# Optimization experiments

Measured on AMD Instinct MI355X. Metric: run time of the kernel, lower is better.

## Reference

```python
import jax, jax.numpy as jnp
import numpy as np

PAD = 0
SOS = 1
NEG = -1e9


def _lstm_scan(x, Wih, Whh, b, h0, c0, reverse=False):
    # x: [T, B, in]; torch gate order i, f, g, o
    def step(carry, xt):
        h, c = carry
        g = xt @ Wih.T + h @ Whh.T + b
        i, f, gg, o = jnp.split(g, 4, axis=-1)
        c = jax.nn.sigmoid(f) * c + jax.nn.sigmoid(i) * jnp.tanh(gg)
        h = jax.nn.sigmoid(o) * jnp.tanh(c)
        return (h, c), h
    (hT, cT), hs = jax.lax.scan(step, (h0, c0), x, reverse=reverse)
    return hs, hT, cT


def setup_inputs() -> dict:
    B, Ts, Tt = 32, 64, 66
    E, H, V = 512, 512, 16000
    key = jax.random.key(0)
    ks = jax.random.split(key, 16)
    s = 0.05
    n = lambda k, shape: (jax.random.normal(k, shape, dtype=jnp.float32) * s)
    return {
        'src_sentences': jax.random.randint(ks[0], (B, Ts), 4, V),
        'trg_sentences': jax.random.randint(ks[1], (B, Tt), 4, V),
        'src_emb': n(ks[2], (V, E)),
        'trg_emb': n(ks[3], (V, E)),
        'enc0_Wih': n(ks[4], (2, 4 * H, E)),
        'enc0_Whh': n(ks[5], (2, 4 * H, H)),
        'enc0_b': n(ks[6], (2, 4 * H)),
        'enc1_Wih': n(ks[7], (2, 4 * H, 2 * H)),
        'enc1_Whh': n(ks[8], (2, 4 * H, H)),
        'enc1_b': n(ks[9], (2, 4 * H)),
        'dec_Wih': n(ks[10], (8 * H, E)),      # LSTMCell: hidden = 2H -> 4*(2H) gates
        'dec_Whh': n(ks[11], (8 * H, 2 * H)),
        'dec_b': n(ks[12], (8 * H)),
        'out_W1': n(ks[13], (H, 4 * H)),
        'out_W2': n(ks[14], (V - 4, H)),
    }


def reference(src_sentences, trg_sentences, src_emb, trg_emb,
              enc0_Wih, enc0_Whh, enc0_b, enc1_Wih, enc1_Whh, enc1_b,
              dec_Wih, dec_Whh, dec_b, out_W1, out_W2):
    B, Ts = src_sentences.shape
    Tt = trg_sentences.shape[1]
    H = out_W1.shape[0]
    dt = src_emb.dtype
    enc_mask = src_sentences == PAD            # [B, Ts] (all False here)

    # ---- encoder: 2-layer bidirectional LSTM (dropout inactive / eval) ----
    x = jnp.swapaxes(src_emb[src_sentences], 0, 1)   # [Ts, B, E]
    z = jnp.zeros((B, H), dt)
    hf0, hfT, cfT = _lstm_scan(x, enc0_Wih[0], enc0_Whh[0], enc0_b[0], z, z)
    hb0, hbT, cbT = _lstm_scan(x, enc0_Wih[1], enc0_Whh[1], enc0_b[1], z, z, reverse=True)
    x1 = jnp.concatenate([hf0, hb0], axis=-1)        # [Ts, B, 2H]
    hf1, _, _ = _lstm_scan(x1, enc1_Wih[0], enc1_Whh[0], enc1_b[0], z, z)
    hb1, _, _ = _lstm_scan(x1, enc1_Wih[1], enc1_Whh[1], enc1_b[1], z, z, reverse=True)
    enc_out = jnp.swapaxes(jnp.concatenate([hf1, hb1], axis=-1), 0, 1)  # [B, Ts, 2H]
    # module uses encoder_hidden_t[0], [1] -> layer-0 fwd/bwd final states
    hidden = jnp.concatenate([hfT, hbT], axis=-1)    # [B, 2H]
    cell = jnp.concatenate([cfT, cbT], axis=-1)

    # ---- decoder: teacher_force = 1.0 (deterministic) ----
    steps = Tt - 2
    emb_in = jnp.swapaxes(trg_emb[trg_sentences[:, :steps]], 0, 1)  # [steps, B, E]
    tgts = jnp.swapaxes(trg_sentences[:, 1:steps + 1], 0, 1)        # [steps, B]

    def step(carry, inp):
        h, c, loss = carry
        xt, tgt = inp
        g = xt @ dec_Wih.T + h @ dec_Whh.T + dec_b
        i, f, gg, o = jnp.split(g, 4, axis=-1)
        c = jax.nn.sigmoid(f) * c + jax.nn.sigmoid(i) * jnp.tanh(gg)
        h = jax.nn.sigmoid(o) * jnp.tanh(c)
        dmask = tgt == PAD
        h = jnp.where(dmask[:, None], jnp.zeros((), dt), h)  # decoder_hidden_t[mask] = 0
        # dot attention over encoder states
        scores = jnp.einsum('btd,bd->bt', enc_out, h)
        scores = jnp.where(enc_mask, NEG, scores)
        attn = jax.nn.softmax(scores, axis=1)
        ctx = jnp.einsum('bt,btd->bd', attn, enc_out)
        zt = jnp.tanh(jnp.concatenate([h, ctx], axis=-1) @ out_W1.T)
        logits = zt @ out_W2.T                                # [B, V-4]
        logp = jax.nn.log_softmax(logits, axis=1)
        tgt_idx = tgt - 4
        valid = tgt_idx != -4                                 # ignore_index=-4 (PAD)
        safe = jnp.where(valid, tgt_idx, 0)
        nll = -jnp.take_along_axis(logp, safe[:, None], axis=1)[:, 0]
        loss = loss + jnp.sum(jnp.where(valid, nll, jnp.zeros((), dt)))
        pred = jnp.argmax(logits, axis=1) + 4
        return (h, c, loss), pred

    (_, _, loss), preds = jax.lax.scan(step, (hidden, cell, jnp.zeros((), dt)), (emb_in, tgts))
    denom = jnp.sum(trg_sentences[:, 1:-1] != PAD).astype(dt)
    return loss / denom, preds.T  # preds: [B, steps]
```

## Files before the change

### kernel.cpp

```cpp
#include <hip/hip_runtime.h>
#include <hip/hip_bf16.h>
#include <math.h>

#define TSRC 64
#define TTRG 66
#define NVOC 15996
#define NTILE 125

__device__ __forceinline__ float sigm(float x){ return 1.f/(1.f+expf(-x)); }

__global__ __launch_bounds__(256)
void k_gemm128(const float* __restrict__ A, int lda,
               const float* __restrict__ Bw, int ldb,
               const float* __restrict__ bias,
               float* __restrict__ C, int ldc, int K, int nNb)
{
  const int tid = threadIdx.x;
  const int mb = blockIdx.x / nNb;
  const int nb = blockIdx.x % nNb;
  const int m0 = mb*128, n0 = nb*128;

  __shared__ alignas(16) float As[16][132];
  __shared__ alignas(16) float Bs[16][132];
  const int tx = tid & 15;
  const int ty = tid >> 4;
  float acc[8][8];
  #pragma unroll
  for (int i=0;i<8;i++)
    #pragma unroll
    for (int j=0;j<8;j++) acc[i][j]=0.f;

  for (int kt=0; kt<K; kt+=16) {
    #pragma unroll
    for (int i=tid; i<128*16; i+=256) {
      int m = i>>4, k = i&15;
      As[k][m] = A[(size_t)(m0+m)*lda + kt + k];
    }
    #pragma unroll
    for (int i=tid; i<128*16; i+=256) {
      int n = i>>4, k = i&15;
      Bs[k][n] = Bw[(size_t)(n0+n)*ldb + kt + k];
    }
    __syncthreads();
    #pragma unroll
    for (int k=0;k<16;k++) {
      float4 a0 = *reinterpret_cast<const float4*>(&As[k][ty*4]);
      float4 a1 = *reinterpret_cast<const float4*>(&As[k][64+ty*4]);
      float4 b0 = *reinterpret_cast<const float4*>(&Bs[k][tx*4]);
      float4 b1 = *reinterpret_cast<const float4*>(&Bs[k][64+tx*4]);
      float av[8] = {a0.x,a0.y,a0.z,a0.w,a1.x,a1.y,a1.z,a1.w};
      float bv[8] = {b0.x,b0.y,b0.z,b0.w,b1.x,b1.y,b1.z,b1.w};
      #pragma unroll
      for (int i=0;i<8;i++)
        #pragma unroll
        for (int j=0;j<8;j++)
          acc[i][j] = fmaf(av[i], bv[j], acc[i][j]);
    }
    __syncthreads();
  }
  #pragma unroll
  for (int i=0;i<8;i++) {
    int m = m0 + ((i<4) ? ty*4+i : 64+ty*4+(i-4));
    int nA = n0 + tx*4, nB = n0 + 64 + tx*4;
    float4 v0, v1;
    v0.x = acc[i][0] + (bias?bias[nA+0]:0.f);
    v0.y = acc[i][1] + (bias?bias[nA+1]:0.f);
    v0.z = acc[i][2] + (bias?bias[nA+2]:0.f);
    v0.w = acc[i][3] + (bias?bias[nA+3]:0.f);
    v1.x = acc[i][4] + (bias?bias[nB+0]:0.f);
    v1.y = acc[i][5] + (bias?bias[nB+1]:0.f);
    v1.z = acc[i][6] + (bias?bias[nB+2]:0.f);
    v1.w = acc[i][7] + (bias?bias[nB+3]:0.f);
    *reinterpret_cast<float4*>(&C[(size_t)m*ldc + nA]) = v0;
    *reinterpret_cast<float4*>(&C[(size_t)m*ldc + nB]) = v1;
  }
}

__global__ __launch_bounds__(256)
void k_logits(const float* __restrict__ A, const float* __restrict__ Bw,
              const int* __restrict__ trg,
              float* __restrict__ Pmax, int* __restrict__ Parg,
              float* __restrict__ Psum, float* __restrict__ Ltgt)
{
  const int tid = threadIdx.x;
  const int j8   = blockIdx.x & 7;
  const int mb   = (blockIdx.x >> 3) & 15;
  const int nb   = ((blockIdx.x >> 7) << 3) + j8;
  if (nb >= NTILE) return;
  const int m0 = mb*128, n0 = nb*128;

  __shared__ alignas(16) float As[16][132];
  __shared__ alignas(16) float Bs[16][132];
  const int tx = tid & 15;
  const int ty = tid >> 4;
  float acc[8][8];
  #pragma unroll
  for (int i=0;i<8;i++)
    #pragma unroll
    for (int j=0;j<8;j++) acc[i][j]=0.f;

  for (int kt=0; kt<512; kt+=16) {
    #pragma unroll
    for (int i=tid; i<128*16; i+=256) {
      int m = i>>4, k = i&15;
      As[k][m] = A[(size_t)(m0+m)*512 + kt + k];
    }
    #pragma unroll
    for (int i=tid; i<128*16; i+=256) {
      int n = i>>4, k = i&15;
      int gn = n0+n;
      Bs[k][n] = (gn < NVOC) ? Bw[(size_t)gn*512 + kt + k] : 0.f;
    }
    __syncthreads();
    #pragma unroll
    for (int k=0;k<16;k++) {
      float4 a0 = *reinterpret_cast<const float4*>(&As[k][ty*4]);
      float4 a1 = *reinterpret_cast<const float4*>(&As[k][64+ty*4]);
      float4 b0 = *reinterpret_cast<const float4*>(&Bs[k][tx*4]);
      float4 b1 = *reinterpret_cast<const float4*>(&Bs[k][64+tx*4]);
      float av[8] = {a0.x,a0.y,a0.z,a0.w,a1.x,a1.y,a1.z,a1.w};
      float bv[8] = {b0.x,b0.y,b0.z,b0.w,b1.x,b1.y,b1.z,b1.w};
      #pragma unroll
      for (int i=0;i<8;i++)
        #pragma unroll
        for (int j=0;j<8;j++)
          acc[i][j] = fmaf(av[i], bv[j], acc[i][j]);
    }
    __syncthreads();
  }

  #pragma unroll
  for (int i=0;i<8;i++) {
    int r = m0 + ((i<4) ? ty*4+i : 64+ty*4+(i-4));
    int step = r >> 5, b = r & 31;
    int tgt = trg[b*TTRG + step + 1];
    int ti = tgt - 4;
    float m = -3.4e38f; int am = 0x7fffffff;
    #pragma unroll
    for (int j=0;j<8;j++) {
      int gn = n0 + ((j<4) ? tx*4+j : 64+tx*4+(j-4));
      if (gn < NVOC) {
        float x = acc[i][j];
        if (x > m || (x == m && gn < am)) { m = x; am = gn; }
      }
    }
    float s = 0.f;
    float lt = 0.f;
    #pragma unroll
    for (int j=0;j<8;j++) {
      int gn = n0 + ((j<4) ? tx*4+j : 64+tx*4+(j-4));
      if (gn < NVOC) {
        s += expf(acc[i][j] - m);
        if (gn == ti) lt = acc[i][j];
      }
    }
    #pragma unroll
    for (int d=1; d<16; d<<=1) {
      float m2 = __shfl_xor(m, d);
      int   a2 = __shfl_xor(am, d);
      float s2 = __shfl_xor(s, d);
      float l2 = __shfl_xor(lt, d);
      float M = fmaxf(m, m2);
      s = s*expf(m - M) + s2*expf(m2 - M);
      if (m2 > m || (m2 == m && a2 < am)) am = a2;
      m = M;
      lt += l2;
    }
    if (tx == 0) {
      size_t pi = (size_t)r*NTILE + nb;
      Pmax[pi] = m; Parg[pi] = am; Psum[pi] = s;
      if (ti >= n0 && ti < n0 + 128) Ltgt[r] = lt;
    }
  }
}

struct GArgs {
  const float* A;  int lda;
  const float* Bw; int ldb;
  const float* bias;
  float* C; int ldc;
  int N; int K; int nNb; int act;
};

template<int BM,int BN,int BK,int TM,int TN>
__global__ __launch_bounds__(256)
void k_gemm(GArgs a)
{
  const int tid = threadIdx.x;
  const int mb = blockIdx.x / a.nNb;
  const int nb = blockIdx.x % a.nNb;
  const int m0 = mb*BM, n0 = nb*BN;
  const float* A  = a.A + (size_t)m0*a.lda;
  const float* Bw = a.Bw;

  __shared__ float As[BK][BM+1];
  __shared__ float Bs[BK][BN+4];
  const int tx = tid % (BN/TN);
  const int ty = tid / (BN/TN);
  float acc[TM][TN];
  #pragma unroll
  for (int i=0;i<TM;i++)
    #pragma unroll
    for (int j=0;j<TN;j++) acc[i][j]=0.f;

  for (int kt=0; kt<a.K; kt+=BK) {
    #pragma unroll
    for (int i=tid; i<BM*BK; i+=256) {
      int m = i/BK, k = i%BK;
      As[k][m] = A[(size_t)m*a.lda + kt + k];
    }
    #pragma unroll
    for (int i=tid; i<BN*BK; i+=256) {
      int n = i/BK, k = i%BK;
      int gn = n0+n;
      Bs[k][n] = (gn < a.N) ? Bw[(size_t)gn*a.ldb + kt + k] : 0.f;
    }
    __syncthreads();
    #pragma unroll
    for (int k=0;k<BK;k++) {
      float av[TM], bv[TN];
      #pragma unroll
      for (int i=0;i<TM;i++) av[i]=As[k][ty*TM+i];
      #pragma unroll
      for (int j=0;j<TN;j++) bv[j]=Bs[k][tx*TN+j];
      #pragma unroll
      for (int i=0;i<TM;i++)
        #pragma unroll
        for (int j=0;j<TN;j++)
          acc[i][j] = fmaf(av[i], bv[j], acc[i][j]);
    }
    __syncthreads();
  }
  #pragma unroll
  for (int i=0;i<TM;i++) {
    int m = m0 + ty*TM + i;
    #pragma unroll
    for (int j=0;j<TN;j++) {
      int n = n0 + tx*TN + j;
      if (n < a.N) {
        float v = acc[i][j];
        if (a.bias) v += a.bias[n];
        if (a.act)  v = tanhf(v);
        a.C[(size_t)m*a.ldc + n] = v;
      }
    }
  }
}

__global__ __launch_bounds__(128)
void k_combine(const float* __restrict__ Pmax, const int* __restrict__ Parg,
               const float* __restrict__ Psum, const float* __restrict__ Ltgt,
               const int* __restrict__ trg,
               float* __restrict__ nll, float* __restrict__ outp)
{
  int r = blockIdx.x;
  int step = r >> 5, b = r & 31;
  int tid = threadIdx.x;
  __shared__ float sm[128]; __shared__ int sa[128]; __shared__ float ssum[128];
  float m = -3.4e38f; int am = 0x7fffffff; float s = 0.f;
  if (tid < NTILE) {
    size_t pi = (size_t)r*NTILE + tid;
    m = Pmax[pi]; am = Parg[pi]; s = Psum[pi];
  }
  sm[tid]=m; sa[tid]=am; ssum[tid]=s; __syncthreads();
  for (int off=64; off; off>>=1) {
    if (tid < off) {
      float m2 = sm[tid+off]; int a2 = sa[tid+off]; float s2 = ssum[tid+off];
      float m1 = sm[tid];     int a1 = sa[tid];     float s1 = ssum[tid];
      float M = fmaxf(m1, m2);
      ssum[tid] = s1*expf(m1 - M) + s2*expf(m2 - M);
      if (m2 > m1 || (m2 == m1 && a2 < a1)) sa[tid] = a2;
      sm[tid] = M;
    }
    __syncthreads();
  }
  if (tid == 0) {
    int tgt = trg[b*TTRG + step + 1];
    float nl = 0.f;
    if (tgt != 0) nl = -(Ltgt[r] - sm[0] - logf(ssum[0]));
    nll[step*32 + b] = nl;
    outp[1 + b*64 + step] = (float)(sa[0] + 4);
  }
}

__global__ void k_gather(const float* __restrict__ emb, const int* __restrict__ tok,
                         float* __restrict__ outp, int Tfull)
{
  int r = blockIdx.x;
  int t = r >> 5, b = r & 31;
  int token = tok[b*Tfull + t];
  const float4* s = (const float4*)(emb + (size_t)token*512);
  float4* d = (float4*)(outp + (size_t)r*512);
  d[threadIdx.x] = s[threadIdx.x];
}

__global__ __launch_bounds__(256)
void k_estep(const float* __restrict__ Whh,
             const float* __restrict__ xg,
             const float* __restrict__ hin,
             float* __restrict__ hout,
             float* __restrict__ cst,
             float* __restrict__ xout, int s, int mode)
{
  const int bid = blockIdx.x;
  const int dir = bid >> 7;
  const int j0  = (bid & 127) * 4;
  const int tid = threadIdx.x;
  const int kg  = tid >> 5;
  const int b   = tid & 31;
  __shared__ float4 wl4[16*128];
  __shared__ float red[4*16*33];

  {
    const float* W = Whh + (size_t)dir*2048*512;
    for (int idx = tid; idx < 16*128; idx += 256) {
      int r = idx >> 7, c = idx & 127;
      int g = r >> 2, jj = r & 3;
      wl4[idx] = ((const float4*)(W + (size_t)(g*512 + j0 + jj)*512))[c];
    }
  }
  float4 hreg[16];
  {
    const float4* H4 = (const float4*)(hin + (size_t)dir*32*512);
    #pragma unroll
    for (int j=0;j<16;j++) hreg[j] = H4[(size_t)b*128 + kg*16 + j];
  }
  __syncthreads();

  float acc[16];
  #pragma unroll
  for (int r=0;r<16;r++) {
    const float4* wr = wl4 + r*128 + kg*16;
    float a0=0.f,a1=0.f,a2=0.f,a3=0.f;
    #pragma unroll
    for (int j=0;j<16;j++) {
      float4 w = wr[j];
      a0 = fmaf(w.x, hreg[j].x, a0);
      a1 = fmaf(w.y, hreg[j].y, a1);
      a2 = fmaf(w.z, hreg[j].z, a2);
      a3 = fmaf(w.w, hreg[j].w, a3);
    }
    acc[r] = (a0+a1)+(a2+a3);
  }
  #pragma unroll
  for (int r=0;r<16;r++) acc[r] += __shfl_xor(acc[r], 32);
  const int wv = tid >> 6;
  if ((tid & 32) == 0) {
    #pragma unroll
    for (int r=0;r<16;r++) red[wv*528 + r*33 + b] = acc[r];
  }
  __syncthreads();

  if (tid < 128) {
    int jj = tid >> 5, bb = tid & 31;
    int jh = j0 + jj;
    int t  = dir ? (63 - s) : s;
    const float* x = xg + ((size_t)t*32 + bb)*4096 + dir*2048;
    float g4[4];
    #pragma unroll
    for (int g=0; g<4; g++) {
      int r = g*4 + jj;
      g4[g] = ((red[0*528 + r*33 + bb] + red[1*528 + r*33 + bb])
             + (red[2*528 + r*33 + bb] + red[3*528 + r*33 + bb]))
             + x[g*512 + jh];
    }
    size_t ci = ((size_t)dir*32 + bb)*512 + jh;
    float cn = sigm(g4[1])*cst[ci] + sigm(g4[0])*tanhf(g4[2]);
    float hn = sigm(g4[3])*tanhf(cn);
    cst[ci] = cn;
    hout[ci] = hn;
    if (mode == 0) xout[((size_t)t*32 + bb)*1024 + dir*512 + jh] = hn;
    else           xout[((size_t)bb*64 + t)*1024 + dir*512 + jh] = hn;
  }
}

__global__ __launch_bounds__(256)
void k_dstep(const float* __restrict__ Whh,
             const float* __restrict__ xg_t,
             const float* __restrict__ hin,
             float* __restrict__ cst,
             float* __restrict__ hall_t,
             const int* __restrict__ trg, int st)
{
  const int bid = blockIdx.x;
  const int j0  = bid*4;
  const int tid = threadIdx.x;
  const int kg  = tid >> 5;
  const int b   = tid & 31;
  __shared__ float4 wl4[8*256];
  __shared__ float red[4*16*33];

  float4 hreg[32];
  {
    const float4* H4 = (const float4*)hin;
    #pragma unroll
    for (int j=0;j<32;j++) hreg[j] = H4[(size_t)b*256 + kg*32 + j];
  }

  float acc[16];
  #pragma unroll
  for (int hh=0; hh<2; hh++) {
    for (int idx = tid; idx < 8*256; idx += 256) {
      int rl = idx >> 8, c = idx & 255;
      int r = hh*8 + rl;
      int g = r >> 2, jj = r & 3;
      wl4[idx] = ((const float4*)(Whh + (size_t)(g*1024 + j0 + jj)*1024))[c];
    }
    __syncthreads();
    #pragma unroll
    for (int rl=0; rl<8; rl++) {
      const float4* wr = wl4 + rl*256 + kg*32;
      float a0=0.f,a1=0.f,a2=0.f,a3=0.f;
      #pragma unroll
      for (int j=0;j<32;j++) {
        float4 w = wr[j];
        a0 = fmaf(w.x, hreg[j].x, a0);
        a1 = fmaf(w.y, hreg[j].y, a1);
        a2 = fmaf(w.z, hreg[j].z, a2);
        a3 = fmaf(w.w, hreg[j].w, a3);
      }
      acc[hh*8 + rl] = (a0+a1)+(a2+a3);
    }
    __syncthreads();
  }
  #pragma unroll
  for (int r=0;r<16;r++) acc[r] += __shfl_xor(acc[r], 32);
  const int wv = tid >> 6;
  if ((tid & 32) == 0) {
    #pragma unroll
    for (int r=0;r<16;r++) red[wv*528 + r*33 + b] = acc[r];
  }
  __syncthreads();

  if (tid < 128) {
    int jj = tid >> 5, bb = tid & 31;
    int jh = j0 + jj;
    int tgt = trg[bb*TTRG + st + 1];
    bool dm = (tgt == 0);
    const float* x = xg_t + (size_t)bb*4096;
    float g4[4];
    #pragma unroll
    for (int g=0; g<4; g++) {
      int r = g*4 + jj;
      g4[g] = ((red[0*528 + r*33 + bb] + red[1*528 + r*33 + bb])
             + (red[2*528 + r*33 + bb] + red[3*528 + r*33 + bb]))
             + x[g*1024 + jh];
    }
    size_t ci = (size_t)bb*1024 + jh;
    float cn = sigm(g4[1])*cst[ci] + sigm(g4[0])*tanhf(g4[2]);
    float hn = sigm(g4[3])*tanhf(cn);
    cst[ci] = cn;
    hall_t[ci] = dm ? 0.f : hn;
  }
}

__global__ void k_pack(const float* __restrict__ hfin, const float* __restrict__ cfin,
                       float* __restrict__ dh, float* __restrict__ dcc)
{
  int tid = blockIdx.x*256 + threadIdx.x;
  int j = tid & 1023, b = tid >> 10;
  int dir = j >> 9, jj = j & 511;
  size_t si = ((size_t)dir*32 + b)*512 + jj;
  dh[(size_t)b*1024 + j]  = hfin[si];
  dcc[(size_t)b*1024 + j] = cfin[si];
}

__global__ __launch_bounds__(256)
void k_attn(const float* __restrict__ Hall,
            const float* __restrict__ encout,
            const int* __restrict__ src,
            float* __restrict__ hctx)
{
  int bid = blockIdx.x;
  int t = bid >> 5, b = bid & 31;
  int tid = threadIdx.x;
  __shared__ float sh[1024];
  __shared__ float ssc[64];
  const float* h = Hall + ((size_t)t*32 + b)*1024;
  size_t row = (size_t)t*32 + b;
  #pragma unroll
  for (int r=0;r<4;r++) {
    int jh = tid + 256*r;
    float v = h[jh];
    sh[jh] = v;
    hctx[row*2048 + jh] = v;
  }
  __syncthreads();
  {
    int tq = tid >> 2, part = tid & 3;
    const float* eo = encout + ((size_t)b*64 + tq)*1024 + part*256;
    const float* hh = sh + part*256;
    float s = 0.f;
    for (int k=0;k<256;k++) s = fmaf(hh[k], eo[k], s);
    s += __shfl_xor(s, 1);
    s += __shfl_xor(s, 2);
    if (part == 0) ssc[tq] = (src[b*TSRC + tq] == 0) ? -1e9f : s;
  }
  __syncthreads();
  if (tid < 64) {
    float v = ssc[tid];
    float m = v;
    for (int d=1; d<64; d<<=1) m = fmaxf(m, __shfl_xor(m, d));
    float e = expf(v - m);
    float su = e;
    for (int d=1; d<64; d<<=1) su += __shfl_xor(su, d);
    ssc[tid] = e / su;
  }
  __syncthreads();
  #pragma unroll
  for (int r=0;r<4;r++) {
    int k = tid + 256*r;
    float a = 0.f;
    const float* eb = encout + (size_t)b*65536 + k;
    for (int tt=0;tt<64;tt++) a = fmaf(ssc[tt], eb[tt*1024], a);
    hctx[row*2048 + 1024 + k] = a;
  }
}

__global__ __launch_bounds__(256)
void k_final(const float* __restrict__ nll, const int* __restrict__ trg,
             float* __restrict__ outp)
{
  int tid = threadIdx.x;
  __shared__ float ss[256]; __shared__ int sc[256];
  float s = 0.f; int cnt = 0;
  for (int i=tid; i<2048; i+=256) {
    s += nll[i];
    int b = i >> 6, t = (i & 63) + 1;
    cnt += (trg[b*TTRG + t] != 0);
  }
  ss[tid]=s; sc[tid]=cnt; __syncthreads();
  for (int off=128; off; off>>=1) {
    if (tid<off) { ss[tid]+=ss[tid+off]; sc[tid]+=sc[tid+off]; }
    __syncthreads();
  }
  if (tid==0) outp[0] = ss[0] / (float)sc[0];
}

static void launch_big(hipStream_t st, const float* A, int lda,
                       const float* Bw, int ldb, const float* bias,
                       float* C, int ldc, int M, int N, int K)
{
  int nNb = N/128;
  dim3 g((M/128)*nNb, 1, 1);
  k_gemm128<<<g, dim3(256), 0, st>>>(A, lda, Bw, ldb, bias, C, ldc, K, nNb);
}

static void launch_med(hipStream_t st, const float* A, int lda,
                       const float* Bw, int ldb, const float* bias,
                       float* C, int ldc, int M, int N, int K, int act)
{
  GArgs a;
  a.A=A; a.lda=lda;
  a.Bw=Bw; a.ldb=ldb;
  a.bias=bias;
  a.C=C; a.ldc=ldc;
  a.N=N; a.K=K; a.nNb=(N+63)/64; a.act=act;
  dim3 g((M/64)*a.nNb, 1, 1);
  k_gemm<64,64,16,4,4><<<g, dim3(256), 0, st>>>(a);
}

extern "C" void kernel_launch(void* const* d_in, const int* in_sizes, int n_in,
                              void* d_out, int out_size, void* d_ws, size_t ws_size,
                              hipStream_t stream)
{
  (void)in_sizes; (void)n_in; (void)out_size; (void)ws_size;
  const int*   src   = (const int*)  d_in[0];
  const int*   trg   = (const int*)  d_in[1];
  const float* semb  = (const float*)d_in[2];
  const float* temb  = (const float*)d_in[3];
  const float* e0Wih = (const float*)d_in[4];
  const float* e0Whh = (const float*)d_in[5];
  const float* e0b   = (const float*)d_in[6];
  const float* e1Wih = (const float*)d_in[7];
  const float* e1Whh = (const float*)d_in[8];
  const float* e1b   = (const float*)d_in[9];
  const float* dWih  = (const float*)d_in[10];
  const float* dWhh  = (const float*)d_in[11];
  const float* db    = (const float*)d_in[12];
  const float* W1    = (const float*)d_in[13];
  const float* W2    = (const float*)d_in[14];
  float* out = (float*)d_out;

  float* ws = (float*)d_ws;
  size_t o = 0;
  float* x_in   = ws + o; o += (size_t)2048*512;
  float* xg     = ws + o; o += (size_t)2048*4096;
  float* x1     = ws + o; o += (size_t)2048*1024;
  float* encout = ws + o; o += (size_t)2048*1024;
  float* hA     = ws + o; o += 2*32*512;
  float* hB     = ws + o; o += 2*32*512;
  float* cbuf   = ws + o; o += 2*32*512;
  float* dh0    = ws + o; o += 32*1024;
  float* dc     = ws + o; o += 32*1024;
  float* nll    = ws + o; o += 2048;
  float* Hall   = x1;
  float* hctx   = xg;
  float* zt     = x_in;
  float* Pmax   = xg + (size_t)4*1024*1024;
  int*   Parg   = (int*)(Pmax + (size_t)2048*NTILE);
  float* Psum   = Pmax + (size_t)2*2048*NTILE;
  float* Ltgt   = Pmax + (size_t)3*2048*NTILE;

  hipMemsetAsync(hA,   0, 2*32*512*sizeof(float), stream);
  hipMemsetAsync(cbuf, 0, 2*32*512*sizeof(float), stream);
  k_gather<<<dim3(2048), dim3(128), 0, stream>>>(semb, src, x_in, TSRC);
  launch_big(stream, x_in, 512, e0Wih, 512, e0b, xg, 4096, 2048, 4096, 512);
  for (int s=0; s<64; s++) {
    float* hin  = (s&1) ? hB : hA;
    float* hout = (s&1) ? hA : hB;
    k_estep<<<dim3(256), dim3(256), 0, stream>>>(e0Whh, xg, hin, hout, cbuf, x1, s, 0);
  }
  k_pack<<<dim3(128), dim3(256), 0, stream>>>(hA, cbuf, dh0, dc);

  hipMemsetAsync(hA,   0, 2*32*512*sizeof(float), stream);
  hipMemsetAsync(cbuf, 0, 2*32*512*sizeof(float), stream);
  launch_big(stream, x1, 1024, e1Wih, 1024, e1b, xg, 4096, 2048, 4096, 1024);
  for (int s=0; s<64; s++) {
    float* hin  = (s&1) ? hB : hA;
    float* hout = (s&1) ? hA : hB;
    k_estep<<<dim3(256), dim3(256), 0, stream>>>(e1Whh, xg, hin, hout, cbuf, encout, s, 1);
  }

  k_gather<<<dim3(2048), dim3(128), 0, stream>>>(temb, trg, x_in, TTRG);
  launch_big(stream, x_in, 512, dWih, 512, db, xg, 4096, 2048, 4096, 512);
  for (int st=0; st<64; st++) {
    const float* hin = (st == 0) ? dh0 : (Hall + (size_t)(st-1)*32*1024);
    k_dstep<<<dim3(256), dim3(256), 0, stream>>>(dWhh, xg + (size_t)st*32*4096,
                 hin, dc, Hall + (size_t)st*32*1024, trg, st);
  }

  k_attn<<<dim3(2048), dim3(256), 0, stream>>>(Hall, encout, src, hctx);
  launch_med(stream, hctx, 2048, W1, 2048, nullptr, zt, 512, 2048, 512, 2048, 1);
  k_logits<<<dim3(2048), dim3(256), 0, stream>>>(zt, W2, trg, Pmax, Parg, Psum, Ltgt);
  k_combine<<<dim3(2048), dim3(128), 0, stream>>>(Pmax, Parg, Psum, Ltgt, trg, nll, out);
  k_final<<<dim3(1), dim3(256), 0, stream>>>(nll, trg, out);
}
```

Measured before the change: 4.118 ms.

## Fuse encoder layer-1 and decoder recurrent steps into one concurrent kernel

The decoder recurrence depends only on layer-0 final states and target embeddings, so it is now run alongside the encoder layer-1 recurrence in a single 512-block launch per step. Encoder blocks take the first 256 block ids and decoder blocks the rest. This halves the number of serial step launches and lets the two recurrences share the GPU. The decoder input projection (x·Wih) is computed inside each step instead of by a separate large GEMM, which adds per-step weight loads and FMAs to every decoder step.

```diff
diff --git a/kernel.cpp b/kernel.cpp
--- a/kernel.cpp
+++ b/kernel.cpp
@@ -300,7 +300,7 @@
              const float* __restrict__ hin,
              float* __restrict__ hout,
              float* __restrict__ cst,
-             float* __restrict__ xout, int s, int mode)
+             float* __restrict__ xout, int s)
 {
   const int bid = blockIdx.x;
   const int dir = bid >> 7;
@@ -369,88 +369,184 @@
     float hn = sigm(g4[3])*tanhf(cn);
     cst[ci] = cn;
     hout[ci] = hn;
-    if (mode == 0) xout[((size_t)t*32 + bb)*1024 + dir*512 + jh] = hn;
-    else           xout[((size_t)bb*64 + t)*1024 + dir*512 + jh] = hn;
+    xout[((size_t)t*32 + bb)*1024 + dir*512 + jh] = hn;
   }
 }
 
 __global__ __launch_bounds__(256)
-void k_dstep(const float* __restrict__ Whh,
-             const float* __restrict__ xg_t,
-             const float* __restrict__ hin,
-             float* __restrict__ cst,
-             float* __restrict__ hall_t,
-             const int* __restrict__ trg, int st)
-{
-  const int bid = blockIdx.x;
-  const int j0  = bid*4;
+void k_mstep(const float* __restrict__ eWhh,
+             const float* __restrict__ xg,
+             const float* __restrict__ ehin, float* __restrict__ ehout,
+             float* __restrict__ ecst,
+             float* __restrict__ encout,
+             const float* __restrict__ dWhh,
+             const float* __restrict__ dWih,
+             const float* __restrict__ db,
+             const float* __restrict__ xemb,
+             const float* __restrict__ dhin,
+             float* __restrict__ dcst,
+             float* __restrict__ dhall_t,
+             const int* __restrict__ trg, int s)
+{
   const int tid = threadIdx.x;
   const int kg  = tid >> 5;
   const int b   = tid & 31;
-  __shared__ float4 wl4[8*256];
+  __shared__ float4 wl4[2048];
   __shared__ float red[4*16*33];
 
-  float4 hreg[32];
-  {
-    const float4* H4 = (const float4*)hin;
-    #pragma unroll
-    for (int j=0;j<32;j++) hreg[j] = H4[(size_t)b*256 + kg*32 + j];
-  }
-
-  float acc[16];
-  #pragma unroll
-  for (int hh=0; hh<2; hh++) {
-    for (int idx = tid; idx < 8*256; idx += 256) {
-      int rl = idx >> 8, c = idx & 255;
-      int r = hh*8 + rl;
-      int g = r >> 2, jj = r & 3;
-      wl4[idx] = ((const float4*)(Whh + (size_t)(g*1024 + j0 + jj)*1024))[c];
-    }
-    __syncthreads();
-    #pragma unroll
-    for (int rl=0; rl<8; rl++) {
-      const float4* wr = wl4 + rl*256 + kg*32;
+  if (blockIdx.x < 256) {
+    const int dir = blockIdx.x >> 7;
+    const int j0  = (blockIdx.x & 127) * 4;
+    {
+      const float* W = eWhh + (size_t)dir*2048*512;
+      for (int idx = tid; idx < 16*128; idx += 256) {
+        int r = idx >> 7, c = idx & 127;
+        int g = r >> 2, jj = r & 3;
+        wl4[idx] = ((const float4*)(W + (size_t)(g*512 + j0 + jj)*512))[c];
+      }
+    }
+    float4 hreg[16];
+    {
+      const float4* H4 = (const float4*)(ehin + (size_t)dir*32*512);
+      #pragma unroll
+      for (int j=0;j<16;j++) hreg[j] = H4[(size_t)b*128 + kg*16 + j];
+    }
+    __syncthreads();
+
+    float acc[16];
+    #pragma unroll
+    for (int r=0;r<16;r++) {
+      const float4* wr = wl4 + r*128 + kg*16;
       float a0=0.f,a1=0.f,a2=0.f,a3=0.f;
       #pragma unroll
-      for (int j=0;j<32;j++) {
+      for (int j=0;j<16;j++) {
         float4 w = wr[j];
         a0 = fmaf(w.x, hreg[j].x, a0);
         a1 = fmaf(w.y, hreg[j].y, a1);
         a2 = fmaf(w.z, hreg[j].z, a2);
         a3 = fmaf(w.w, hreg[j].w, a3);
       }
-      acc[hh*8 + rl] = (a0+a1)+(a2+a3);
-    }
-    __syncthreads();
-  }
-  #pragma unroll
-  for (int r=0;r<16;r++) acc[r] += __shfl_xor(acc[r], 32);
-  const int wv = tid >> 6;
-  if ((tid & 32) == 0) {
-    #pragma unroll
-    for (int r=0;r<16;r++) red[wv*528 + r*33 + b] = acc[r];
-  }
-  __syncthreads();
-
-  if (tid < 128) {
-    int jj = tid >> 5, bb = tid & 31;
-    int jh = j0 + jj;
-    int tgt = trg[bb*TTRG + st + 1];
-    bool dm = (tgt == 0);
-    const float* x = xg_t + (size_t)bb*4096;
-    float g4[4];
-    #pragma unroll
-    for (int g=0; g<4; g++) {
-      int r = g*4 + jj;
-      g4[g] = ((red[0*528 + r*33 + bb] + red[1*528 + r*33 + bb])
-             + (red[2*528 + r*33 + bb] + red[3*528 + r*33 + bb]))
-             + x[g*1024 + jh];
-    }
-    size_t ci = (size_t)bb*1024 + jh;
-    float cn = sigm(g4[1])*cst[ci] + sigm(g4[0])*tanhf(g4[2]);
-    float hn = sigm(g4[3])*tanhf(cn);
-    cst[ci] = cn;
-    hall_t[ci] = dm ? 0.f : hn;
+      acc[r] = (a0+a1)+(a2+a3);
+    }
+    #pragma unroll
+    for (int r=0;r<16;r++) acc[r] += __shfl_xor(acc[r], 32);
+    const int wv = tid >> 6;
+    if ((tid & 32) == 0) {
+      #pragma unroll
+      for (int r=0;r<16;r++) red[wv*528 + r*33 + b] = acc[r];
+    }
+    __syncthreads();
+
+    if (tid < 128) {
+      int jj = tid >> 5, bb = tid & 31;
+      int jh = j0 + jj;
+      int t  = dir ? (63 - s) : s;
+      const float* x = xg + ((size_t)t*32 + bb)*4096 + dir*2048;
+      float g4[4];
+      #pragma unroll
+      for (int g=0; g<4; g++) {
+        int r = g*4 + jj;
+        g4[g] = ((red[0*528 + r*33 + bb] + red[1*528 + r*33 + bb])
+               + (red[2*528 + r*33 + bb] + red[3*528 + r*33 + bb]))
+               + x[g*512 + jh];
+      }
+      size_t ci = ((size_t)dir*32 + bb)*512 + jh;
+      float cn = sigm(g4[1])*ecst[ci] + sigm(g4[0])*tanhf(g4[2]);
+      float hn = sigm(g4[3])*tanhf(cn);
+      ecst[ci] = cn;
+      ehout[ci] = hn;
+      encout[((size_t)bb*64 + t)*1024 + dir*512 + jh] = hn;
+    }
+  } else {
+    const int j0 = (blockIdx.x - 256) * 4;
+    for (int idx = tid; idx < 16*128; idx += 256) {
+      int r = idx >> 7, c = idx & 127;
+      int g = r >> 2, jj = r & 3;
+      wl4[idx] = ((const float4*)(dWih + (size_t)(g*1024 + j0 + jj)*512))[c];
+    }
+    float4 xreg[16];
+    {
+      const float4* X4 = (const float4*)(xemb + (size_t)s*32*512);
+      #pragma unroll
+      for (int j=0;j<16;j++) xreg[j] = X4[(size_t)b*128 + kg*16 + j];
+    }
+    float4 hreg[32];
+    {
+      const float4* H4 = (const float4*)dhin;
+      #pragma unroll
+      for (int j=0;j<32;j++) hreg[j] = H4[(size_t)b*256 + kg*32 + j];
+    }
+    __syncthreads();
+
+    float acc[16];
+    #pragma unroll
+    for (int r=0;r<16;r++) {
+      const float4* wr = wl4 + r*128 + kg*16;
+      float a0=0.f,a1=0.f,a2=0.f,a3=0.f;
+      #pragma unroll
+      for (int j=0;j<16;j++) {
+        float4 w = wr[j];
+        a0 = fmaf(w.x, xreg[j].x, a0);
+        a1 = fmaf(w.y, xreg[j].y, a1);
+        a2 = fmaf(w.z, xreg[j].z, a2);
+        a3 = fmaf(w.w, xreg[j].w, a3);
+      }
+      acc[r] = (a0+a1)+(a2+a3);
+    }
+    __syncthreads();
+    #pragma unroll
+    for (int hh=0; hh<2; hh++) {
+      for (int idx = tid; idx < 8*256; idx += 256) {
+        int rl = idx >> 8, c = idx & 255;
+        int r = hh*8 + rl;
+        int g = r >> 2, jj = r & 3;
+        wl4[idx] = ((const float4*)(dWhh + (size_t)(g*1024 + j0 + jj)*1024))[c];
+      }
+      __syncthreads();
+      #pragma unroll
+      for (int rl=0; rl<8; rl++) {
+        const float4* wr = wl4 + rl*256 + kg*32;
+        float a0=0.f,a1=0.f,a2=0.f,a3=0.f;
+        #pragma unroll
+        for (int j=0;j<32;j++) {
+          float4 w = wr[j];
+          a0 = fmaf(w.x, hreg[j].x, a0);
+          a1 = fmaf(w.y, hreg[j].y, a1);
+          a2 = fmaf(w.z, hreg[j].z, a2);
+          a3 = fmaf(w.w, hreg[j].w, a3);
+        }
+        acc[hh*8 + rl] += (a0+a1)+(a2+a3);
+      }
+      __syncthreads();
+    }
+    #pragma unroll
+    for (int r=0;r<16;r++) acc[r] += __shfl_xor(acc[r], 32);
+    const int wv = tid >> 6;
+    if ((tid & 32) == 0) {
+      #pragma unroll
+      for (int r=0;r<16;r++) red[wv*528 + r*33 + b] = acc[r];
+    }
+    __syncthreads();
+
+    if (tid < 128) {
+      int jj = tid >> 5, bb = tid & 31;
+      int jh = j0 + jj;
+      int tgt = trg[bb*TTRG + s + 1];
+      bool dm = (tgt == 0);
+      float g4[4];
+      #pragma unroll
+      for (int g=0; g<4; g++) {
+        int r = g*4 + jj;
+        g4[g] = ((red[0*528 + r*33 + bb] + red[1*528 + r*33 + bb])
+               + (red[2*528 + r*33 + bb] + red[3*528 + r*33 + bb]))
+               + db[g*1024 + jh];
+      }
+      size_t ci = (size_t)bb*1024 + jh;
+      float cn = sigm(g4[1])*dcst[ci] + sigm(g4[0])*tanhf(g4[2]);
+      float hn = sigm(g4[3])*tanhf(cn);
+      dcst[ci] = cn;
+      dhall_t[ci] = dm ? 0.f : hn;
+    }
   }
 }
 
@@ -609,25 +705,22 @@
   for (int s=0; s<64; s++) {
     float* hin  = (s&1) ? hB : hA;
     float* hout = (s&1) ? hA : hB;
-    k_estep<<<dim3(256), dim3(256), 0, stream>>>(e0Whh, xg, hin, hout, cbuf, x1, s, 0);
+    k_estep<<<dim3(256), dim3(256), 0, stream>>>(e0Whh, xg, hin, hout, cbuf, x1, s);
   }
   k_pack<<<dim3(128), dim3(256), 0, stream>>>(hA, cbuf, dh0, dc);
 
   hipMemsetAsync(hA,   0, 2*32*512*sizeof(float), stream);
   hipMemsetAsync(cbuf, 0, 2*32*512*sizeof(float), stream);
   launch_big(stream, x1, 1024, e1Wih, 1024, e1b, xg, 4096, 2048, 4096, 1024);
+  k_gather<<<dim3(2048), dim3(128), 0, stream>>>(temb, trg, x_in, TTRG);
+
   for (int s=0; s<64; s++) {
-    float* hin  = (s&1) ? hB : hA;
-    float* hout = (s&1) ? hA : hB;
-    k_estep<<<dim3(256), dim3(256), 0, stream>>>(e1Whh, xg, hin, hout, cbuf, encout, s, 1);
-  }
-
-  k_gather<<<dim3(2048), dim3(128), 0, stream>>>(temb, trg, x_in, TTRG);
-  launch_big(stream, x_in, 512, dWih, 512, db, xg, 4096, 2048, 4096, 512);
-  for (int st=0; st<64; st++) {
-    const float* hin = (st == 0) ? dh0 : (Hall + (size_t)(st-1)*32*1024);
-    k_dstep<<<dim3(256), dim3(256), 0, stream>>>(dWhh, xg + (size_t)st*32*4096,
-                 hin, dc, Hall + (size_t)st*32*1024, trg, st);
+    float* ehin  = (s&1) ? hB : hA;
+    float* ehout = (s&1) ? hA : hB;
+    const float* dhin = (s == 0) ? dh0 : (Hall + (size_t)(s-1)*32*1024);
+    k_mstep<<<dim3(512), dim3(256), 0, stream>>>(
+        e1Whh, xg, ehin, ehout, cbuf, encout,
+        dWhh, dWih, db, x_in, dhin, dc, Hall + (size_t)s*32*1024, trg, s);
   }
 
   k_attn<<<dim3(2048), dim3(256), 0, stream>>>(Hall, encout, src, hctx);
```

After: 4.742 ms. +15.1%, slower.

## Double-buffer shared-memory tiles in fp32 GEMM and logits kernels

Applied to the files above, without the earlier changes.

Both tiled fp32 GEMM kernels (the generic one and the fused vocabulary-logits one) now keep two shared-memory stages. The next K-slice is prefetched into registers while the current slice is multiplied, then written to the other buffer. This halves the barriers per K step and hides global-load latency behind the FMA loop. The cost is doubled LDS use and 16 extra registers per thread, which may lower occupancy.

```diff
diff --git a/kernel.cpp b/kernel.cpp
--- a/kernel.cpp
+++ b/kernel.cpp
@@ -20,34 +20,45 @@
   const int nb = blockIdx.x % nNb;
   const int m0 = mb*128, n0 = nb*128;
 
-  __shared__ alignas(16) float As[16][132];
-  __shared__ alignas(16) float Bs[16][132];
+  __shared__ alignas(16) float As[2][16][132];
+  __shared__ alignas(16) float Bs[2][16][132];
   const int tx = tid & 15;
   const int ty = tid >> 4;
+  const int sm_ = tid >> 4;
+  const int sk_ = tid & 15;
   float acc[8][8];
   #pragma unroll
   for (int i=0;i<8;i++)
     #pragma unroll
     for (int j=0;j<8;j++) acc[i][j]=0.f;
 
-  for (int kt=0; kt<K; kt+=16) {
-    #pragma unroll
-    for (int i=tid; i<128*16; i+=256) {
-      int m = i>>4, k = i&15;
-      As[k][m] = A[(size_t)(m0+m)*lda + kt + k];
-    }
-    #pragma unroll
-    for (int i=tid; i<128*16; i+=256) {
-      int n = i>>4, k = i&15;
-      Bs[k][n] = Bw[(size_t)(n0+n)*ldb + kt + k];
-    }
-    __syncthreads();
+  #pragma unroll
+  for (int q=0;q<8;q++) {
+    int m = sm_ + 16*q;
+    As[0][sk_][m] = A[(size_t)(m0+m)*lda + sk_];
+    Bs[0][sk_][m] = Bw[(size_t)(n0+m)*ldb + sk_];
+  }
+  __syncthreads();
+
+  const int NT = K >> 4;
+  for (int t=0; t<NT; ++t) {
+    int cur = t & 1, nxt = cur^1;
+    float aR[8], bR[8];
+    if (t+1 < NT) {
+      int kt = (t+1)<<4;
+      #pragma unroll
+      for (int q=0;q<8;q++) {
+        int m = sm_ + 16*q;
+        aR[q] = A[(size_t)(m0+m)*lda + kt + sk_];
+        bR[q] = Bw[(size_t)(n0+m)*ldb + kt + sk_];
+      }
+    }
     #pragma unroll
     for (int k=0;k<16;k++) {
-      float4 a0 = *reinterpret_cast<const float4*>(&As[k][ty*4]);
-      float4 a1 = *reinterpret_cast<const float4*>(&As[k][64+ty*4]);
-      float4 b0 = *reinterpret_cast<const float4*>(&Bs[k][tx*4]);
-      float4 b1 = *reinterpret_cast<const float4*>(&Bs[k][64+tx*4]);
+      float4 a0 = *reinterpret_cast<const float4*>(&As[cur][k][ty*4]);
+      float4 a1 = *reinterpret_cast<const float4*>(&As[cur][k][64+ty*4]);
+      float4 b0 = *reinterpret_cast<const float4*>(&Bs[cur][k][tx*4]);
+      float4 b1 = *reinterpret_cast<const float4*>(&Bs[cur][k][64+tx*4]);
       float av[8] = {a0.x,a0.y,a0.z,a0.w,a1.x,a1.y,a1.z,a1.w};
       float bv[8] = {b0.x,b0.y,b0.z,b0.w,b1.x,b1.y,b1.z,b1.w};
       #pragma unroll
@@ -55,6 +66,14 @@
         #pragma unroll
         for (int j=0;j<8;j++)
           acc[i][j] = fmaf(av[i], bv[j], acc[i][j]);
+    }
+    if (t+1 < NT) {
+      #pragma unroll
+      for (int q=0;q<8;q++) {
+        int m = sm_ + 16*q;
+        As[nxt][sk_][m] = aR[q];
+        Bs[nxt][sk_][m] = bR[q];
+      }
     }
     __syncthreads();
   }
@@ -89,35 +108,46 @@
   if (nb >= NTILE) return;
   const int m0 = mb*128, n0 = nb*128;
 
-  __shared__ alignas(16) float As[16][132];
-  __shared__ alignas(16) float Bs[16][132];
+  __shared__ alignas(16) float As[2][16][132];
+  __shared__ alignas(16) float Bs[2][16][132];
   const int tx = tid & 15;
   const int ty = tid >> 4;
+  const int sm_ = tid >> 4;
+  const int sk_ = tid & 15;
   float acc[8][8];
   #pragma unroll
   for (int i=0;i<8;i++)
     #pragma unroll
     for (int j=0;j<8;j++) acc[i][j]=0.f;
 
-  for (int kt=0; kt<512; kt+=16) {
-    #pragma unroll
-    for (int i=tid; i<128*16; i+=256) {
-      int m = i>>4, k = i&15;
-      As[k][m] = A[(size_t)(m0+m)*512 + kt + k];
-    }
-    #pragma unroll
-    for (int i=tid; i<128*16; i+=256) {
-      int n = i>>4, k = i&15;
-      int gn = n0+n;
-      Bs[k][n] = (gn < NVOC) ? Bw[(size_t)gn*512 + kt + k] : 0.f;
-    }
-    __syncthreads();
+  #pragma unroll
+  for (int q=0;q<8;q++) {
+    int m = sm_ + 16*q;
+    int gn = n0 + m;
+    As[0][sk_][m] = A[(size_t)(m0+m)*512 + sk_];
+    Bs[0][sk_][m] = (gn < NVOC) ? Bw[(size_t)gn*512 + sk_] : 0.f;
+  }
+  __syncthreads();
+
+  for (int t=0; t<32; ++t) {
+    int cur = t & 1, nxt = cur^1;
+    float aR[8], bR[8];
+    if (t+1 < 32) {
+      int kt = (t+1)<<4;
+      #pragma unroll
+      for (int q=0;q<8;q++) {
+        int m = sm_ + 16*q;
+        int gn = n0 + m;
+        aR[q] = A[(size_t)(m0+m)*512 + kt + sk_];
+        bR[q] = (gn < NVOC) ? Bw[(size_t)gn*512 + kt + sk_] : 0.f;
+      }
+    }
     #pragma unroll
     for (int k=0;k<16;k++) {
-      float4 a0 = *reinterpret_cast<const float4*>(&As[k][ty*4]);
-      float4 a1 = *reinterpret_cast<const float4*>(&As[k][64+ty*4]);
-      float4 b0 = *reinterpret_cast<const float4*>(&Bs[k][tx*4]);
-      float4 b1 = *reinterpret_cast<const float4*>(&Bs[k][64+tx*4]);
+      float4 a0 = *reinterpret_cast<const float4*>(&As[cur][k][ty*4]);
+      float4 a1 = *reinterpret_cast<const float4*>(&As[cur][k][64+ty*4]);
+      float4 b0 = *reinterpret_cast<const float4*>(&Bs[cur][k][tx*4]);
+      float4 b1 = *reinterpret_cast<const float4*>(&Bs[cur][k][64+tx*4]);
       float av[8] = {a0.x,a0.y,a0.z,a0.w,a1.x,a1.y,a1.z,a1.w};
       float bv[8] = {b0.x,b0.y,b0.z,b0.w,b1.x,b1.y,b1.z,b1.w};
       #pragma unroll
@@ -125,6 +155,14 @@
         #pragma unroll
         for (int j=0;j<8;j++)
           acc[i][j] = fmaf(av[i], bv[j], acc[i][j]);
+    }
+    if (t+1 < 32) {
+      #pragma unroll
+      for (int q=0;q<8;q++) {
+        int m = sm_ + 16*q;
+        As[nxt][sk_][m] = aR[q];
+        Bs[nxt][sk_][m] = bR[q];
+      }
     }
     __syncthreads();
   }
```

New measurement: 4.406 ms. 1.07x slower.
